# Kernel optimization log

Hardware: AMD Instinct MI355X
Metric: run time of the kernel (lower is better)

Reference implementation:

```python
import jax, jax.numpy as jnp
import numpy as np

B, S, E, H = 2, 2048, 1024, 16
D = E // H  # head size = 64


def setup_inputs() -> dict:
    key = jax.random.key(0)
    ks = jax.random.split(key, 13)
    scale = 1.0 / np.sqrt(E)
    inp = {
        "q": jax.random.normal(ks[0], (B, S, E), jnp.float32),
        "k": jax.random.normal(ks[1], (B, S, E), jnp.float32),
        "v": jax.random.normal(ks[2], (B, S, E), jnp.float32),
        "mask": jax.random.randint(ks[3], (B, 1, S, S), 0, 2, jnp.int32),
        "Wq": jax.random.normal(ks[4], (E, E), jnp.float32) * scale,
        "bq": jnp.zeros((E,), jnp.float32),
        "Wk": jax.random.normal(ks[5], (E, E), jnp.float32) * scale,
        "bk": jnp.zeros((E,), jnp.float32),
        "Wv": jax.random.normal(ks[6], (E, E), jnp.float32) * scale,
        "bv": jnp.zeros((E,), jnp.float32),
        "Wo": jax.random.normal(ks[7], (E, E), jnp.float32) * scale,
        "bo": jnp.zeros((E,), jnp.float32),
    }
    return inp


def reference(q, k, v, mask, Wq, bq, Wk, bk, Wv, bv, Wo, bo):
    # Linear projections (torch Linear: x @ W.T + b)
    qh = (q @ Wq.T + bq).reshape(B, S, H, D).transpose(0, 2, 1, 3)  # [B,H,S,D]
    kh = (k @ Wk.T + bk).reshape(B, S, H, D).transpose(0, 2, 1, 3)
    vh = (v @ Wv.T + bv).reshape(B, S, H, D).transpose(0, 2, 1, 3)

    scores = jnp.einsum("bhqd,bhkd->bhqk", qh, kh) / jnp.sqrt(jnp.float32(D))
    scores = jnp.where(mask == 0, jnp.float32(-1e10), scores)
    attn = jax.nn.softmax(scores, axis=-1)  # [B,H,S,S]
    ctx = jnp.einsum("bhqk,bhkd->bhqd", attn, vh)  # dropout p=0.0 -> identity

    out = ctx.transpose(0, 2, 1, 3).reshape(B, S, E)
    return out @ Wo.T + bo
```

## Files before the change

### kernel.cpp

```cpp
#include <hip/hip_runtime.h>

typedef unsigned short ushort_t;
typedef __attribute__((ext_vector_type(8))) short short8;
typedef __attribute__((ext_vector_type(4))) float f32x4;
typedef __attribute__((ext_vector_type(4))) unsigned short ushort4_t;
typedef __attribute__((ext_vector_type(4))) unsigned int uint4_t;

#define BB 2
#define SS 2048
#define EE 1024
#define HH 16
#define DD 64
#define MM (BB*SS)

#define QB_OFF  0u
#define KB_OFF  4194304u
#define VB_OFF  8388608u
#define WQ_OFF  12582912u
#define WK_OFF  13631488u
#define WV_OFF  14680064u
#define WO_OFF  15728640u
#define QH_OFF  16777216u
#define KH_OFF  20971520u
#define VT_OFF  25165824u
#define CTX_OFF QB_OFF
#define MB_OFF  29360128u

__device__ __forceinline__ ushort_t f2bf(float x) {
    unsigned u = __builtin_bit_cast(unsigned, x);
    u += 0x7FFFu + ((u >> 16) & 1u);
    return (ushort_t)(u >> 16);
}

__device__ __forceinline__ unsigned pk_bf16(float a, float b) {
    unsigned ua = __builtin_bit_cast(unsigned, a);
    unsigned ub = __builtin_bit_cast(unsigned, b);
    ua += 0x7FFFu + ((ua >> 16) & 1u);
    ub += 0x7FFFu + ((ub >> 16) & 1u);
    return __builtin_amdgcn_perm(ub, ua, 0x07060302u);
}

__device__ __forceinline__ void load_lds16(const void* g, void* l) {
    __builtin_amdgcn_global_load_lds((const __attribute__((address_space(1))) void*)g,
                                     (__attribute__((address_space(3))) void*)l, 16, 0, 0);
}

__global__ __launch_bounds__(256) void prep_kernel(
    const float* __restrict__ q, const float* __restrict__ k, const float* __restrict__ v,
    const int* __restrict__ mask,
    const float* __restrict__ Wq, const float* __restrict__ Wk,
    const float* __restrict__ Wv, const float* __restrict__ Wo,
    ushort_t* __restrict__ wsb, unsigned* __restrict__ maskbits)
{
    int g = blockIdx.x;
    if (g < 16384) {
        int idx = g * 256 + threadIdx.x;
        const float* src; ushort_t* dst; int rel;
        if      (idx < 1048576) { src = q;  dst = wsb + QB_OFF; rel = idx; }
        else if (idx < 2097152) { src = k;  dst = wsb + KB_OFF; rel = idx - 1048576; }
        else if (idx < 3145728) { src = v;  dst = wsb + VB_OFF; rel = idx - 2097152; }
        else if (idx < 3407872) { src = Wq; dst = wsb + WQ_OFF; rel = idx - 3145728; }
        else if (idx < 3670016) { src = Wk; dst = wsb + WK_OFF; rel = idx - 3407872; }
        else if (idx < 3932160) { src = Wv; dst = wsb + WV_OFF; rel = idx - 3670016; }
        else                    { src = Wo; dst = wsb + WO_OFF; rel = idx - 3932160; }
        f32x4 val = ((const f32x4*)src)[rel];
        ushort4_t o;
        o.x = f2bf(val.x); o.y = f2bf(val.y); o.z = f2bf(val.z); o.w = f2bf(val.w);
        ((ushort4_t*)dst)[rel] = o;
    } else {
        int t = (g - 16384) * 256 + threadIdx.x;
        int b   = t >> 17;
        int rem = t & 131071;
        int w   = rem >> 11;
        int sk  = rem & 2047;
        unsigned bits = 0;
        const int* mp = mask + ((size_t)b * SS + (size_t)w * 32) * SS + sk;
        #pragma unroll
        for (int jj = 0; jj < 32; ++jj)
            bits |= (mp[(size_t)jj * SS] != 0 ? 1u : 0u) << jj;
        maskbits[((size_t)b * SS + sk) * 64 + w] = bits;
    }
}

__device__ __forceinline__ void gemm_mainloop(
    const ushort_t* __restrict__ A, const ushort_t* __restrict__ Bm,
    int m0, int n0, f32x4 acc[4][4], ushort_t* As, ushort_t* Bs)
{
    const int tid  = threadIdx.x;
    const int wave = tid >> 6, lane = tid & 63;
    const int r16  = lane >> 2;
    const int c8   = (lane & 3) * 8;
    const int lane15 = lane & 15, quad = lane >> 4;
    const int wm = wave >> 1, wn = wave & 1;

    #pragma unroll 1
    for (int kt = 0; kt < 32; ++kt) {
        const int k0 = kt * 32;
        __syncthreads();
        const ushort_t* ga = A  + (size_t)(m0 + wave * 32 + r16) * 1024 + k0 + c8;
        load_lds16(ga,             As + wave * 1024);
        load_lds16(ga + 16 * 1024, As + wave * 1024 + 512);
        const ushort_t* gb = Bm + (size_t)(n0 + wave * 32 + r16) * 1024 + k0 + c8;
        load_lds16(gb,             Bs + wave * 1024);
        load_lds16(gb + 16 * 1024, Bs + wave * 1024 + 512);
        __syncthreads();

        short8 a[4], bf[4];
        #pragma unroll
        for (int i = 0; i < 4; ++i)
            a[i] = *(const short8*)&As[(wm * 64 + i * 16 + lane15) * 32 + quad * 8];
        #pragma unroll
        for (int j = 0; j < 4; ++j)
            bf[j] = *(const short8*)&Bs[(wn * 64 + j * 16 + lane15) * 32 + quad * 8];
        #pragma unroll
        for (int i = 0; i < 4; ++i)
            #pragma unroll
            for (int j = 0; j < 4; ++j)
                acc[i][j] = __builtin_amdgcn_mfma_f32_16x16x32_bf16(a[i], bf[j], acc[i][j], 0, 0, 0);
    }
}

__global__ __launch_bounds__(256) void gemm_qkv(
    ushort_t* __restrict__ wsb,
    const float* __restrict__ bq, const float* __restrict__ bk, const float* __restrict__ bv)
{
    __shared__ ushort_t As[128 * 32], Bs[128 * 32];
    const int z = blockIdx.z;
    const ushort_t* A;
    const ushort_t* Bm;
    if      (z == 0) { A = wsb + QB_OFF; Bm = wsb + WQ_OFF; }
    else if (z == 1) { A = wsb + KB_OFF; Bm = wsb + WK_OFF; }
    else             { A = wsb + WV_OFF; Bm = wsb + VB_OFF; }
    const float* bias  = (z == 0) ? bq : (z == 1) ? bk : bv;
    ushort_t* dst      = wsb + (z == 0 ? QH_OFF : z == 1 ? KH_OFF : VT_OFF);
    const int m0 = (z < 2) ? blockIdx.y * 128 : blockIdx.x * 128;
    const int n0 = (z < 2) ? blockIdx.x * 128 : blockIdx.y * 128;

    f32x4 acc[4][4];
    #pragma unroll
    for (int i = 0; i < 4; ++i)
        #pragma unroll
        for (int j = 0; j < 4; ++j) acc[i][j] = (f32x4){0.f, 0.f, 0.f, 0.f};

    gemm_mainloop(A, Bm, m0, n0, acc, As, Bs);

    const int tid = threadIdx.x, wave = tid >> 6, lane = tid & 63;
    const int lane15 = lane & 15, quad = lane >> 4;
    const int wm = wave >> 1, wn = wave & 1;
    const float scale = (z == 0) ? 0.180336880111f : 1.0f;

    if (z < 2) {
        #pragma unroll
        for (int i = 0; i < 4; ++i) {
            #pragma unroll
            for (int j = 0; j < 4; ++j) {
                int col = n0 + wn * 64 + j * 16 + lane15;
                float bv_ = bias[col];
                int hh = col >> 6, d = col & 63;
                #pragma unroll
                for (int r = 0; r < 4; ++r) {
                    int row = m0 + wm * 64 + i * 16 + quad * 4 + r;
                    int bb = row >> 11, s = row & 2047;
                    float val = (acc[i][j][r] + bv_) * scale;
                    dst[(((size_t)bb * HH + hh) * SS + s) * DD + d] = f2bf(val);
                }
            }
        }
    } else {
        #pragma unroll
        for (int i = 0; i < 4; ++i) {
            #pragma unroll
            for (int r = 0; r < 4; ++r) {
                int row = m0 + wm * 64 + i * 16 + quad * 4 + r;
                float bv_ = bias[row];
                int hh = row >> 6, d = row & 63;
                #pragma unroll
                for (int j = 0; j < 4; ++j) {
                    int col = n0 + wn * 64 + j * 16 + lane15;
                    int bb = col >> 11, s = col & 2047;
                    int kk = s & 127;
                    int sp = ((kk & 15) << 3) + (kk >> 4);
                    dst[(((size_t)bb * HH + hh) * DD + d) * SS + (s & ~127) + sp]
                        = f2bf(acc[i][j][r] + bv_);
                }
            }
        }
    }
}

__global__ __launch_bounds__(256, 2) void attn_kernel(
    const ushort_t* __restrict__ wsb, const unsigned* __restrict__ maskbits,
    ushort_t* __restrict__ ctx)
{
    __shared__ ushort_t Ks[128 * 64];
    __shared__ ushort_t Vts[64 * 128];
    __shared__ ushort_t Ps[128 * 128];

    const int tid  = threadIdx.x;
    const int wave = tid >> 6, lane = tid & 63;
    const int lane15 = lane & 15, quad = lane >> 4;
    const int sw7 = lane15 & 7;
    const int bh = blockIdx.y;
    const int b  = bh >> 4, h = bh & 15;
    const int q0 = blockIdx.x * 128;

    const ushort_t* Qh  = wsb + QH_OFF;
    const ushort_t* Kh  = wsb + KH_OFF;
    const ushort_t* VhT = wsb + VT_OFF;

    short8 qfrag[2][2];
    #pragma unroll
    for (int i = 0; i < 2; ++i)
        #pragma unroll
        for (int ks = 0; ks < 2; ++ks)
            qfrag[i][ks] = *(const short8*)(Qh +
                ((size_t)bh * SS + q0 + wave * 32 + i * 16 + lane15) * DD + ks * 32 + quad * 8);

    short8 ones_frag;
    {
        short onev = (lane15 == 0) ? (short)0x3F80 : (short)0;
        #pragma unroll
        for (int e = 0; e < 8; ++e) ones_frag[e] = onev;
    }

    const f32x4 zero4 = (f32x4){0.f, 0.f, 0.f, 0.f};
    f32x4 s_acc[2][8];
    f32x4 o_acc[2][4];
    f32x4 osum[2];
    #pragma unroll
    for (int i = 0; i < 2; ++i) {
        #pragma unroll
        for (int jd = 0; jd < 4; ++jd) o_acc[i][jd] = zero4;
        osum[i] = zero4;
    }

    #pragma unroll 1
    for (int kt = 0; kt < 16; ++kt) {
        const int k0 = kt * 128;
        __syncthreads();

        const ushort_t* Kbase = Kh + ((size_t)bh * SS + k0) * DD;
        #pragma unroll
        for (int cc = 0; cc < 4; ++cc) {
            int n = (wave * 4 + cc) * 64 + lane;
            int row = n >> 3;
            int c = (n & 7) ^ (row & 7);
            load_lds16(Kbase + row * 64 + c * 8, Ks + (wave * 4 + cc) * 512);
        }
        const ushort_t* Vbase = VhT + ((size_t)bh * DD) * SS + k0;
        #pragma unroll
        for (int cc = 0; cc < 4; ++cc) {
            int n = (wave * 4 + cc) * 64 + lane;
            int d = n >> 4;
            int c = (n & 15) ^ (d & 7);
            load_lds16(Vbase + (size_t)d * SS + c * 8, Vts + (wave * 4 + cc) * 512);
        }

        unsigned mw[8];
        {
            const int qw = (q0 >> 5) + wave;
            #pragma unroll
            for (int j = 0; j < 8; ++j) {
                int sk = k0 + j * 16 + lane15;
                mw[j] = maskbits[((size_t)b * SS + sk) * 64 + qw];
            }
        }
        __syncthreads();

        #pragma unroll
        for (int j = 0; j < 8; ++j) {
            short8 bf = *(const short8*)&Ks[(j * 16 + lane15) * 64 + ((quad ^ sw7) << 3)];
            s_acc[0][j] = __builtin_amdgcn_mfma_f32_16x16x32_bf16(qfrag[0][0], bf, zero4, 0, 0, 0);
            s_acc[1][j] = __builtin_amdgcn_mfma_f32_16x16x32_bf16(qfrag[1][0], bf, zero4, 0, 0, 0);
        }
        #pragma unroll
        for (int j = 0; j < 8; ++j) {
            short8 bf = *(const short8*)&Ks[(j * 16 + lane15) * 64 + (((4 + quad) ^ sw7) << 3)];
            s_acc[0][j] = __builtin_amdgcn_mfma_f32_16x16x32_bf16(qfrag[0][1], bf, s_acc[0][j], 0, 0, 0);
            s_acc[1][j] = __builtin_amdgcn_mfma_f32_16x16x32_bf16(qfrag[1][1], bf, s_acc[1][j], 0, 0, 0);
        }

        #pragma unroll
        for (int i = 0; i < 2; ++i) {
            #pragma unroll
            for (int r = 0; r < 4; ++r) {
                const int bit = i * 16 + quad * 4 + r;
                float p[8];
                #pragma unroll
                for (int j = 0; j < 8; ++j) {
                    float e = __builtin_amdgcn_exp2f(s_acc[i][j][r]);
                    p[j] = ((mw[j] >> bit) & 1u) ? e : 0.f;
                }
                uint4_t pk;
                pk.x = pk_bf16(p[0], p[1]);
                pk.y = pk_bf16(p[2], p[3]);
                pk.z = pk_bf16(p[4], p[5]);
                pk.w = pk_bf16(p[6], p[7]);
                const int row = wave * 32 + i * 16 + quad * 4 + r;
                *(uint4_t*)&Ps[row * 128 + ((lane15 ^ (row & 7)) << 3)] = pk;
            }
        }

        #pragma unroll
        for (int kb = 0; kb < 4; ++kb) {
            short8 ap[2];
            #pragma unroll
            for (int i = 0; i < 2; ++i)
                ap[i] = *(const short8*)&Ps[(wave * 32 + i * 16 + lane15) * 128 +
                                            (((kb * 4 + quad) ^ sw7) << 3)];
            #pragma unroll
            for (int jd = 0; jd < 4; ++jd) {
                short8 bv_ = *(const short8*)&Vts[(jd * 16 + lane15) * 128 +
                                                  (((kb * 4 + quad) ^ sw7) << 3)];
                o_acc[0][jd] = __builtin_amdgcn_mfma_f32_16x16x32_bf16(ap[0], bv_, o_acc[0][jd], 0, 0, 0);
                o_acc[1][jd] = __builtin_amdgcn_mfma_f32_16x16x32_bf16(ap[1], bv_, o_acc[1][jd], 0, 0, 0);
            }
            osum[0] = __builtin_amdgcn_mfma_f32_16x16x32_bf16(ap[0], ones_frag, osum[0], 0, 0, 0);
            osum[1] = __builtin_amdgcn_mfma_f32_16x16x32_bf16(ap[1], ones_frag, osum[1], 0, 0, 0);
        }
    }

    #pragma unroll
    for (int i = 0; i < 2; ++i) {
        #pragma unroll
        for (int r = 0; r < 4; ++r) {
            float l = __shfl(osum[i][r], lane & 48);
            float inv = 1.0f / l;
            int row = q0 + wave * 32 + i * 16 + quad * 4 + r;
            #pragma unroll
            for (int jd = 0; jd < 4; ++jd) {
                int col = h * DD + jd * 16 + lane15;
                ctx[((size_t)b * SS + row) * EE + col] = f2bf(o_acc[i][jd][r] * inv);
            }
        }
    }
}

__global__ __launch_bounds__(256) void gemm_out(
    const ushort_t* __restrict__ wsb, const float* __restrict__ bo, float* __restrict__ out)
{
    __shared__ ushort_t As[64 * 32];
    __shared__ ushort_t Bs[128 * 32];
    const ushort_t* A  = wsb + CTX_OFF;
    const ushort_t* Bm = wsb + WO_OFF;
    const int m0 = blockIdx.y * 64, n0 = blockIdx.x * 128;

    const int tid = threadIdx.x, wave = tid >> 6, lane = tid & 63;
    const int lane15 = lane & 15, quad = lane >> 4;

    f32x4 acc[8];
    #pragma unroll
    for (int j = 0; j < 8; ++j) acc[j] = (f32x4){0.f, 0.f, 0.f, 0.f};

    #pragma unroll 1
    for (int kt = 0; kt < 32; ++kt) {
        const int k0 = kt * 32;
        __syncthreads();
        {
            int n = wave * 64 + lane;
            load_lds16(A + (size_t)(m0 + (n >> 2)) * 1024 + k0 + (n & 3) * 8,
                       As + wave * 512);
        }
        #pragma unroll
        for (int m = 0; m < 2; ++m) {
            int n = m * 256 + wave * 64 + lane;
            load_lds16(Bm + (size_t)(n0 + (n >> 2)) * 1024 + k0 + (n & 3) * 8,
                       Bs + (m * 256 + wave * 64) * 8);
        }
        __syncthreads();

        short8 a = *(const short8*)&As[(wave * 16 + lane15) * 32 + quad * 8];
        #pragma unroll
        for (int j = 0; j < 8; ++j) {
            short8 bf = *(const short8*)&Bs[(j * 16 + lane15) * 32 + quad * 8];
            acc[j] = __builtin_amdgcn_mfma_f32_16x16x32_bf16(a, bf, acc[j], 0, 0, 0);
        }
    }

    #pragma unroll
    for (int j = 0; j < 8; ++j) {
        int col = n0 + j * 16 + lane15;
        float bv_ = bo[col];
        #pragma unroll
        for (int r = 0; r < 4; ++r) {
            int row = m0 + wave * 16 + quad * 4 + r;
            out[(size_t)row * EE + col] = acc[j][r] + bv_;
        }
    }
}

extern "C" void kernel_launch(void* const* d_in, const int* in_sizes, int n_in,
                              void* d_out, int out_size, void* d_ws, size_t ws_size,
                              hipStream_t stream) {
    const float* q    = (const float*)d_in[0];
    const float* k    = (const float*)d_in[1];
    const float* v    = (const float*)d_in[2];
    const int*   mask = (const int*)  d_in[3];
    const float* Wq   = (const float*)d_in[4];
    const float* bq   = (const float*)d_in[5];
    const float* Wk   = (const float*)d_in[6];
    const float* bk   = (const float*)d_in[7];
    const float* Wv   = (const float*)d_in[8];
    const float* bv   = (const float*)d_in[9];
    const float* Wo   = (const float*)d_in[10];
    const float* bo   = (const float*)d_in[11];

    ushort_t* wsb = (ushort_t*)d_ws;
    unsigned* maskbits = (unsigned*)(wsb + MB_OFF);

    prep_kernel<<<17408, 256, 0, stream>>>(q, k, v, mask, Wq, Wk, Wv, Wo, wsb, maskbits);
    gemm_qkv<<<dim3(8, 32, 3), 256, 0, stream>>>(wsb, bq, bk, bv);
    attn_kernel<<<dim3(16, 32), 256, 0, stream>>>(wsb, maskbits, wsb + CTX_OFF);
    gemm_out<<<dim3(8, 64), 256, 0, stream>>>(wsb, bo, (float*)d_out);
}
```

Measured before the change: 291.9 us.

## Split attention work across 8 waves and vectorize transposed V stores

The attention kernel now runs 512 threads per block, so each wave owns 16 query rows instead of 32. This halves the per-wave accumulator registers and the K/V tile-load share, aiming for more waves in flight to hide latency. Separately, the V-transpose epilogue of the QKV GEMM writes four bf16 values as one vector store, using the permuted key layout directly instead of scattered scalar stores. More waves per block means more barrier participants, and the mask bit indexing now depends on wave parity.

```diff
diff --git a/kernel.cpp b/kernel.cpp
--- a/kernel.cpp
+++ b/kernel.cpp
@@ -167,6 +167,8 @@
             }
         }
     } else {
+        const int bb = n0 >> 11;
+        const int sbase = n0 & 2047;
         #pragma unroll
         for (int i = 0; i < 4; ++i) {
             #pragma unroll
@@ -174,21 +176,17 @@
                 int row = m0 + wm * 64 + i * 16 + quad * 4 + r;
                 float bv_ = bias[row];
                 int hh = row >> 6, d = row & 63;
+                ushort4_t o;
                 #pragma unroll
-                for (int j = 0; j < 4; ++j) {
-                    int col = n0 + wn * 64 + j * 16 + lane15;
-                    int bb = col >> 11, s = col & 2047;
-                    int kk = s & 127;
-                    int sp = ((kk & 15) << 3) + (kk >> 4);
-                    dst[(((size_t)bb * HH + hh) * DD + d) * SS + (s & ~127) + sp]
-                        = f2bf(acc[i][j][r] + bv_);
-                }
-            }
-        }
-    }
-}
-
-__global__ __launch_bounds__(256, 2) void attn_kernel(
+                for (int j = 0; j < 4; ++j) o[j] = f2bf(acc[i][j][r] + bv_);
+                *(ushort4_t*)&dst[(((size_t)bb * HH + hh) * DD + d) * SS
+                                  + sbase + lane15 * 8 + wn * 4] = o;
+            }
+        }
+    }
+}
+
+__global__ __launch_bounds__(512, 4) void attn_kernel(
     const ushort_t* __restrict__ wsb, const unsigned* __restrict__ maskbits,
     ushort_t* __restrict__ ctx)
 {
@@ -208,13 +206,11 @@
     const ushort_t* Kh  = wsb + KH_OFF;
     const ushort_t* VhT = wsb + VT_OFF;
 
-    short8 qfrag[2][2];
-    #pragma unroll
-    for (int i = 0; i < 2; ++i)
-        #pragma unroll
-        for (int ks = 0; ks < 2; ++ks)
-            qfrag[i][ks] = *(const short8*)(Qh +
-                ((size_t)bh * SS + q0 + wave * 32 + i * 16 + lane15) * DD + ks * 32 + quad * 8);
+    short8 qfrag[2];
+    #pragma unroll
+    for (int ks = 0; ks < 2; ++ks)
+        qfrag[ks] = *(const short8*)(Qh +
+            ((size_t)bh * SS + q0 + wave * 16 + lane15) * DD + ks * 32 + quad * 8);
 
     short8 ones_frag;
     {
@@ -224,15 +220,11 @@
     }
 
     const f32x4 zero4 = (f32x4){0.f, 0.f, 0.f, 0.f};
-    f32x4 s_acc[2][8];
-    f32x4 o_acc[2][4];
-    f32x4 osum[2];
-    #pragma unroll
-    for (int i = 0; i < 2; ++i) {
-        #pragma unroll
-        for (int jd = 0; jd < 4; ++jd) o_acc[i][jd] = zero4;
-        osum[i] = zero4;
-    }
+    f32x4 s_acc[8];
+    f32x4 o_acc[4];
+    f32x4 osum = zero4;
+    #pragma unroll
+    for (int jd = 0; jd < 4; ++jd) o_acc[jd] = zero4;
 
     #pragma unroll 1
     for (int kt = 0; kt < 16; ++kt) {
@@ -241,24 +233,24 @@
 
         const ushort_t* Kbase = Kh + ((size_t)bh * SS + k0) * DD;
         #pragma unroll
-        for (int cc = 0; cc < 4; ++cc) {
-            int n = (wave * 4 + cc) * 64 + lane;
+        for (int cc = 0; cc < 2; ++cc) {
+            int n = (wave * 2 + cc) * 64 + lane;
             int row = n >> 3;
             int c = (n & 7) ^ (row & 7);
-            load_lds16(Kbase + row * 64 + c * 8, Ks + (wave * 4 + cc) * 512);
+            load_lds16(Kbase + row * 64 + c * 8, Ks + (wave * 2 + cc) * 512);
         }
         const ushort_t* Vbase = VhT + ((size_t)bh * DD) * SS + k0;
         #pragma unroll
-        for (int cc = 0; cc < 4; ++cc) {
-            int n = (wave * 4 + cc) * 64 + lane;
+        for (int cc = 0; cc < 2; ++cc) {
+            int n = (wave * 2 + cc) * 64 + lane;
             int d = n >> 4;
             int c = (n & 15) ^ (d & 7);
-            load_lds16(Vbase + (size_t)d * SS + c * 8, Vts + (wave * 4 + cc) * 512);
+            load_lds16(Vbase + (size_t)d * SS + c * 8, Vts + (wave * 2 + cc) * 512);
         }
 
         unsigned mw[8];
         {
-            const int qw = (q0 >> 5) + wave;
+            const int qw = (q0 >> 5) + (wave >> 1);
             #pragma unroll
             for (int j = 0; j < 8; ++j) {
                 int sk = k0 + j * 16 + lane15;
@@ -270,68 +262,56 @@
         #pragma unroll
         for (int j = 0; j < 8; ++j) {
             short8 bf = *(const short8*)&Ks[(j * 16 + lane15) * 64 + ((quad ^ sw7) << 3)];
-            s_acc[0][j] = __builtin_amdgcn_mfma_f32_16x16x32_bf16(qfrag[0][0], bf, zero4, 0, 0, 0);
-            s_acc[1][j] = __builtin_amdgcn_mfma_f32_16x16x32_bf16(qfrag[1][0], bf, zero4, 0, 0, 0);
+            s_acc[j] = __builtin_amdgcn_mfma_f32_16x16x32_bf16(qfrag[0], bf, zero4, 0, 0, 0);
         }
         #pragma unroll
         for (int j = 0; j < 8; ++j) {
             short8 bf = *(const short8*)&Ks[(j * 16 + lane15) * 64 + (((4 + quad) ^ sw7) << 3)];
-            s_acc[0][j] = __builtin_amdgcn_mfma_f32_16x16x32_bf16(qfrag[0][1], bf, s_acc[0][j], 0, 0, 0);
-            s_acc[1][j] = __builtin_amdgcn_mfma_f32_16x16x32_bf16(qfrag[1][1], bf, s_acc[1][j], 0, 0, 0);
-        }
-
-        #pragma unroll
-        for (int i = 0; i < 2; ++i) {
-            #pragma unroll
-            for (int r = 0; r < 4; ++r) {
-                const int bit = i * 16 + quad * 4 + r;
-                float p[8];
-                #pragma unroll
-                for (int j = 0; j < 8; ++j) {
-                    float e = __builtin_amdgcn_exp2f(s_acc[i][j][r]);
-                    p[j] = ((mw[j] >> bit) & 1u) ? e : 0.f;
-                }
-                uint4_t pk;
-                pk.x = pk_bf16(p[0], p[1]);
-                pk.y = pk_bf16(p[2], p[3]);
-                pk.z = pk_bf16(p[4], p[5]);
-                pk.w = pk_bf16(p[6], p[7]);
-                const int row = wave * 32 + i * 16 + quad * 4 + r;
-                *(uint4_t*)&Ps[row * 128 + ((lane15 ^ (row & 7)) << 3)] = pk;
-            }
+            s_acc[j] = __builtin_amdgcn_mfma_f32_16x16x32_bf16(qfrag[1], bf, s_acc[j], 0, 0, 0);
+        }
+
+        const int bitbase = (wave & 1) * 16 + quad * 4;
+        #pragma unroll
+        for (int r = 0; r < 4; ++r) {
+            const int bit = bitbase + r;
+            float p[8];
+            #pragma unroll
+            for (int j = 0; j < 8; ++j) {
+                float e = __builtin_amdgcn_exp2f(s_acc[j][r]);
+                p[j] = ((mw[j] >> bit) & 1u) ? e : 0.f;
+            }
+            uint4_t pk;
+            pk.x = pk_bf16(p[0], p[1]);
+            pk.y = pk_bf16(p[2], p[3]);
+            pk.z = pk_bf16(p[4], p[5]);
+            pk.w = pk_bf16(p[6], p[7]);
+            const int row = wave * 16 + quad * 4 + r;
+            *(uint4_t*)&Ps[row * 128 + ((lane15 ^ (row & 7)) << 3)] = pk;
         }
 
         #pragma unroll
         for (int kb = 0; kb < 4; ++kb) {
-            short8 ap[2];
-            #pragma unroll
-            for (int i = 0; i < 2; ++i)
-                ap[i] = *(const short8*)&Ps[(wave * 32 + i * 16 + lane15) * 128 +
+            short8 ap = *(const short8*)&Ps[(wave * 16 + lane15) * 128 +
                                             (((kb * 4 + quad) ^ sw7) << 3)];
             #pragma unroll
             for (int jd = 0; jd < 4; ++jd) {
                 short8 bv_ = *(const short8*)&Vts[(jd * 16 + lane15) * 128 +
                                                   (((kb * 4 + quad) ^ sw7) << 3)];
-                o_acc[0][jd] = __builtin_amdgcn_mfma_f32_16x16x32_bf16(ap[0], bv_, o_acc[0][jd], 0, 0, 0);
-                o_acc[1][jd] = __builtin_amdgcn_mfma_f32_16x16x32_bf16(ap[1], bv_, o_acc[1][jd], 0, 0, 0);
-            }
-            osum[0] = __builtin_amdgcn_mfma_f32_16x16x32_bf16(ap[0], ones_frag, osum[0], 0, 0, 0);
-            osum[1] = __builtin_amdgcn_mfma_f32_16x16x32_bf16(ap[1], ones_frag, osum[1], 0, 0, 0);
-        }
-    }
-
-    #pragma unroll
-    for (int i = 0; i < 2; ++i) {
-        #pragma unroll
-        for (int r = 0; r < 4; ++r) {
-            float l = __shfl(osum[i][r], lane & 48);
-            float inv = 1.0f / l;
-            int row = q0 + wave * 32 + i * 16 + quad * 4 + r;
-            #pragma unroll
-            for (int jd = 0; jd < 4; ++jd) {
-                int col = h * DD + jd * 16 + lane15;
-                ctx[((size_t)b * SS + row) * EE + col] = f2bf(o_acc[i][jd][r] * inv);
-            }
+                o_acc[jd] = __builtin_amdgcn_mfma_f32_16x16x32_bf16(ap, bv_, o_acc[jd], 0, 0, 0);
+            }
+            osum = __builtin_amdgcn_mfma_f32_16x16x32_bf16(ap, ones_frag, osum, 0, 0, 0);
+        }
+    }
+
+    #pragma unroll
+    for (int r = 0; r < 4; ++r) {
+        float l = __shfl(osum[r], lane & 48);
+        float inv = 1.0f / l;
+        int row = q0 + wave * 16 + quad * 4 + r;
+        #pragma unroll
+        for (int jd = 0; jd < 4; ++jd) {
+            int col = h * DD + jd * 16 + lane15;
+            ctx[((size_t)b * SS + row) * EE + col] = f2bf(o_acc[jd][r] * inv);
         }
     }
 }
@@ -410,6 +390,6 @@
 
     prep_kernel<<<17408, 256, 0, stream>>>(q, k, v, mask, Wq, Wk, Wv, Wo, wsb, maskbits);
     gemm_qkv<<<dim3(8, 32, 3), 256, 0, stream>>>(wsb, bq, bk, bv);
-    attn_kernel<<<dim3(16, 32), 256, 0, stream>>>(wsb, maskbits, wsb + CTX_OFF);
+    attn_kernel<<<dim3(16, 32), 512, 0, stream>>>(wsb, maskbits, wsb + CTX_OFF);
     gemm_out<<<dim3(8, 64), 256, 0, stream>>>(wsb, bo, (float*)d_out);
 }
```

New measurement: 292.6 us. Within noise of the previous version (+0.3%).
